# Performance work log

Hardware: AMD Instinct MI355X
Metric: run time of the kernel (lower is better)

The kernel has to match this reference:

```python
import jax, jax.numpy as jnp
import numpy as np

N_HEAD = 16


def setup_inputs() -> dict:
    key = jax.random.key(0)
    k1, k2, k3 = jax.random.split(key, 3)
    B, T, C = 2, 2048, 1024
    x = jax.random.normal(k1, (B, T, C), dtype=jnp.float32)
    w_attn = jax.random.normal(k2, (C, 3 * C), dtype=jnp.float32) * 0.02
    w_proj = jax.random.normal(k3, (C, C), dtype=jnp.float32) * 0.02
    return {"x": x, "w_attn": w_attn, "w_proj": w_proj}


def reference(x, w_attn, w_proj):
    B, T, C = x.shape
    H = N_HEAD
    D = C // H
    qkv = x @ w_attn  # [B, T, 3C]
    q, k, v = jnp.split(qkv, 3, axis=2)
    q = q.reshape(B, T, H, D)
    k = k.reshape(B, T, H, D)
    v = v.reshape(B, T, H, D)
    scale = 1.0 / jnp.sqrt(jnp.asarray(D, dtype=x.dtype))
    # Full T x T score matrix, matching the 'standard_attention' path.
    att = jnp.einsum('bthd,bshd->bhts', q, k) * scale  # [B, H, T, T]
    causal = jnp.tril(jnp.ones((T, T), dtype=bool))
    att = jnp.where(causal[None, None, :, :], att, jnp.asarray(-jnp.inf, dtype=att.dtype))
    att = jax.nn.softmax(att, axis=-1)
    # dropout_p is False (== 0.0) in the original module, so no dropout applied.
    y = jnp.einsum('bhts,bshd->bthd', att, v)  # [B, T, H, D]
    y = y.reshape(B, T, C)
    return y @ w_proj
```

## Files before the change

### kernel.cpp

```cpp
#include <hip/hip_runtime.h>
#include <math.h>

#define BB 2
#define TT 2048
#define HH 16
#define DD 64
#define CC 1024
#define C3 3072

typedef __attribute__((ext_vector_type(8))) short bf16x8;
typedef __attribute__((ext_vector_type(4))) short bf16x4;
typedef __attribute__((ext_vector_type(4))) float f32x4;
typedef __attribute__((ext_vector_type(2))) unsigned int u32x2;

__device__ __forceinline__ unsigned short f2bf(float f) {
  union { float f; unsigned u; } v; v.f = f;
  unsigned r = v.u + 0x7fffu + ((v.u >> 16) & 1u);
  return (unsigned short)(r >> 16);
}
__device__ __forceinline__ unsigned short f2bf_up(float f) {
  union { float f; unsigned u; } v; v.f = f;
  return (unsigned short)((v.u + 0x8000u) >> 16);
}

__device__ __forceinline__ void async_cp16(const void* g, void* l) {
  __builtin_amdgcn_global_load_lds(
      (const __attribute__((address_space(1))) void*)g,
      (__attribute__((address_space(3))) void*)l, 16, 0, 0);
}

__global__ __launch_bounds__(256)
void prep(const float* __restrict__ x, const float* __restrict__ w_attn,
          const float* __restrict__ w_proj, unsigned short* __restrict__ xb,
          unsigned short* __restrict__ wat, unsigned short* __restrict__ wpt) {
  __shared__ __align__(16) float Ts[64][68];
  const int bx = blockIdx.x, tid = threadIdx.x;
  if (bx < 1024) {
    int i = bx * 256 + tid;
#pragma unroll
    for (int it = 0; it < 4; ++it, i += 262144) {
      const float4 v = ((const float4*)x)[i];
      bf16x4 o = {(short)f2bf(v.x), (short)f2bf(v.y),
                  (short)f2bf(v.z), (short)f2bf(v.w)};
      ((bf16x4*)xb)[i] = o;
    }
    return;
  }
  const float* W;
  unsigned short* WT;
  int Nd, bound, n0, k0;
  float s;
  if (bx < 1792) {
    const int bid = bx - 1024;
    W = w_attn; WT = wat; Nd = 3072; bound = 1024; s = 0.18033688f;
    n0 = (bid % 48) * 64; k0 = (bid / 48) * 64;
  } else {
    const int bid = bx - 1792;
    W = w_proj; WT = wpt; Nd = 1024; bound = 0; s = 1.0f;
    n0 = (bid % 16) * 64; k0 = (bid / 16) * 64;
  }
  const int rl = tid >> 4, c4 = tid & 15;
#pragma unroll
  for (int it = 0; it < 4; ++it) {
    const int r = it * 16 + rl;
    *(float4*)&Ts[r][c4 * 4] =
        *(const float4*)(W + (size_t)(k0 + r) * Nd + n0 + c4 * 4);
  }
  __syncthreads();
#pragma unroll
  for (int it = 0; it < 4; ++it) {
    const int n = it * 16 + rl;
    const float sc = (n0 + n < bound) ? s : 1.0f;
    bf16x4 o = {(short)f2bf(Ts[c4 * 4 + 0][n] * sc),
                (short)f2bf(Ts[c4 * 4 + 1][n] * sc),
                (short)f2bf(Ts[c4 * 4 + 2][n] * sc),
                (short)f2bf(Ts[c4 * 4 + 3][n] * sc)};
    *(bf16x4*)(WT + (size_t)(n0 + n) * CC + k0 + c4 * 4) = o;
  }
}

__global__ __launch_bounds__(256, 2)
void gemm_qkv(const unsigned short* __restrict__ A,
              const unsigned short* __restrict__ BT,
              unsigned short* __restrict__ Cb,
              unsigned short* __restrict__ Vout) {
  __shared__ __align__(16) unsigned short As[2 * 128 * 32];
  __shared__ __align__(16) unsigned short Bs[2 * 192 * 32];

  const int tid = threadIdx.x;
  const int w = tid >> 6, lane = tid & 63;
  const int l15 = lane & 15, quad = lane >> 4;
  const int row0 = blockIdx.y * 128, col0 = blockIdx.x * 192;

  const int ca0 = tid, ca1 = tid + 256;
  const int ra0 = ca0 >> 2, ka0 = ((ca0 & 3) ^ ((ca0 >> 3) & 3)) * 8;
  const int ra1 = ca1 >> 2, ka1 = ((ca1 & 3) ^ ((ca1 >> 3) & 3)) * 8;
  const unsigned short* gA0 = A + (size_t)(row0 + ra0) * CC + ka0;
  const unsigned short* gA1 = A + (size_t)(row0 + ra1) * CC + ka1;
  const int cb0 = tid, cb1 = tid + 256, cb2 = tid + 512;
  const int rb0 = cb0 >> 2, kb0 = ((cb0 & 3) ^ ((cb0 >> 3) & 3)) * 8;
  const int rb1 = cb1 >> 2, kb1 = ((cb1 & 3) ^ ((cb1 >> 3) & 3)) * 8;
  const int rb2 = cb2 >> 2, kb2 = ((cb2 & 3) ^ ((cb2 >> 3) & 3)) * 8;
  const unsigned short* gB0 = BT + (size_t)(col0 + rb0) * CC + kb0;
  const unsigned short* gB1 = BT + (size_t)(col0 + rb1) * CC + kb1;
  const unsigned short* gB2 = BT + (size_t)(col0 + rb2) * CC + kb2;
  const int la0 = tid * 16, la1 = tid * 16 + 4096;
  const int lb0 = tid * 16, lb1 = tid * 16 + 4096, lb2 = tid * 16 + 8192;

  const int fro = l15 * 64 + 16 * (quad ^ ((l15 >> 1) & 3));

  f32x4 acc[8][3];
#pragma unroll
  for (int i = 0; i < 8; ++i)
#pragma unroll
    for (int j = 0; j < 3; ++j) acc[i][j] = (f32x4){0.f, 0.f, 0.f, 0.f};

  async_cp16(gA0, (char*)As + la0);
  async_cp16(gA1, (char*)As + la1);
  async_cp16(gB0, (char*)Bs + lb0);
  async_cp16(gB1, (char*)Bs + lb1);
  async_cp16(gB2, (char*)Bs + lb2);

  for (int i = 0; i < 32; ++i) {
    const int cur = i & 1;
    __syncthreads();

    if (i + 1 < 32) {
      const int k1 = (i + 1) * 32;
      const int ab = (cur ^ 1) * 8192, bb = (cur ^ 1) * 12288;
      async_cp16(gA0 + k1, (char*)As + ab + la0);
      async_cp16(gA1 + k1, (char*)As + ab + la1);
      async_cp16(gB0 + k1, (char*)Bs + bb + lb0);
      async_cp16(gB1 + k1, (char*)Bs + bb + lb1);
      async_cp16(gB2 + k1, (char*)Bs + bb + lb2);
    }

    const char* fA = (const char*)As + cur * 8192 + fro;
    const char* fB = (const char*)Bs + cur * 12288 + w * 3072 + fro;

    bf16x8 af[8], bf[3];
#pragma unroll
    for (int mt = 0; mt < 8; ++mt) af[mt] = *(const bf16x8*)(fA + mt * 1024);
#pragma unroll
    for (int nt = 0; nt < 3; ++nt) bf[nt] = *(const bf16x8*)(fB + nt * 1024);
#pragma unroll
    for (int mt = 0; mt < 8; ++mt)
#pragma unroll
      for (int nt = 0; nt < 3; ++nt)
        acc[mt][nt] = __builtin_amdgcn_mfma_f32_16x16x32_bf16(
            af[mt], bf[nt], acc[mt][nt], 0, 0, 0);
  }

#pragma unroll
  for (int mt = 0; mt < 8; ++mt) {
    const int rbase = row0 + mt * 16 + quad * 4;
#pragma unroll
    for (int nt = 0; nt < 3; ++nt) {
      const int colb = col0 + w * 48 + nt * 16;
      if (colb >= 2048) {
        const int bq = rbase >> 11, t0 = rbase & 2047;
        const int d = colb + l15 - 2048;
        bf16x4 o = {(short)f2bf(acc[mt][nt][0]), (short)f2bf(acc[mt][nt][1]),
                    (short)f2bf(acc[mt][nt][2]), (short)f2bf(acc[mt][nt][3])};
        *(bf16x4*)(Vout + (((size_t)(bq << 10) + d) << 11) + t0) = o;
      } else {
        const int col = colb + l15;
#pragma unroll
        for (int r = 0; r < 4; ++r)
          Cb[(size_t)(rbase + r) * C3 + col] = f2bf(acc[mt][nt][r]);
      }
    }
  }
}

__global__ __launch_bounds__(256, 2)
void gemm_out(const unsigned short* __restrict__ A,
              const unsigned short* __restrict__ BT,
              float* __restrict__ Cf) {
  __shared__ __align__(16) unsigned short As[2 * 64 * 64];
  __shared__ __align__(16) unsigned short Bs[2 * 128 * 64];

  const int tid = threadIdx.x;
  const int w = tid >> 6, lane = tid & 63;
  const int l15 = lane & 15, quad = lane >> 4;
  const int wm = w >> 1, wn = w & 1;
  const int row0 = blockIdx.y * 64, col0 = blockIdx.x * 128;

  const int ca0 = tid, ca1 = tid + 256;
  const int ra0 = ca0 >> 3, ka0 = ((ca0 & 7) ^ ((ca0 >> 3) & 7)) * 8;
  const int ra1 = ca1 >> 3, ka1 = ((ca1 & 7) ^ ((ca1 >> 3) & 7)) * 8;
  const unsigned short* gA0 = A + (size_t)(row0 + ra0) * CC + ka0;
  const unsigned short* gA1 = A + (size_t)(row0 + ra1) * CC + ka1;
  const unsigned short* gB[4];
  int lb[4];
#pragma unroll
  for (int t = 0; t < 4; ++t) {
    const int c = tid + t * 256;
    const int rb = c >> 3, kb = ((c & 7) ^ ((c >> 3) & 7)) * 8;
    gB[t] = BT + (size_t)(col0 + rb) * CC + kb;
    lb[t] = c * 16;
  }
  const int la0 = tid * 16, la1 = tid * 16 + 4096;

  const int fro = l15 * 128 + ((quad ^ (l15 & 7)) << 4);

  f32x4 acc[2][4];
#pragma unroll
  for (int i = 0; i < 2; ++i)
#pragma unroll
    for (int j = 0; j < 4; ++j) acc[i][j] = (f32x4){0.f, 0.f, 0.f, 0.f};

  async_cp16(gA0, (char*)As + la0);
  async_cp16(gA1, (char*)As + la1);
#pragma unroll
  for (int t = 0; t < 4; ++t) async_cp16(gB[t], (char*)Bs + lb[t]);

  for (int i = 0; i < 16; ++i) {
    const int cur = i & 1;
    __syncthreads();

    if (i + 1 < 16) {
      const int k1 = (i + 1) * 64;
      const int ab = (cur ^ 1) * 8192, bb = (cur ^ 1) * 16384;
      async_cp16(gA0 + k1, (char*)As + ab + la0);
      async_cp16(gA1 + k1, (char*)As + ab + la1);
#pragma unroll
      for (int t = 0; t < 4; ++t) async_cp16(gB[t] + k1, (char*)Bs + bb + lb[t]);
    }

    const char* fA = (const char*)As + cur * 8192 + wm * 4096 + fro;
    const char* fB = (const char*)Bs + cur * 16384 + wn * 8192 + fro;

#pragma unroll
    for (int kh = 0; kh < 2; ++kh) {
      const int xo = kh * 64;
      bf16x8 af[2], bf[4];
#pragma unroll
      for (int mt = 0; mt < 2; ++mt)
        af[mt] = *(const bf16x8*)(fA + mt * 2048 + ((fro + xo) & 127) - (fro & 127));
#pragma unroll
      for (int nt = 0; nt < 4; ++nt)
        bf[nt] = *(const bf16x8*)(fB + nt * 2048 + ((fro + xo) & 127) - (fro & 127));
#pragma unroll
      for (int mt = 0; mt < 2; ++mt)
#pragma unroll
        for (int nt = 0; nt < 4; ++nt)
          acc[mt][nt] = __builtin_amdgcn_mfma_f32_16x16x32_bf16(
              af[mt], bf[nt], acc[mt][nt], 0, 0, 0);
    }
  }

#pragma unroll
  for (int mt = 0; mt < 2; ++mt) {
    const int rbase = row0 + wm * 32 + mt * 16 + quad * 4;
#pragma unroll
    for (int r = 0; r < 4; ++r) {
      float* cr = Cf + (size_t)(rbase + r) * CC + col0 + wn * 64 + l15;
#pragma unroll
      for (int nt = 0; nt < 4; ++nt) cr[nt * 16] = acc[mt][nt][r];
    }
  }
}

__global__ __launch_bounds__(256)
void attn_mfma(const unsigned short* __restrict__ qkvb,
               const unsigned short* __restrict__ vt,
               unsigned short* __restrict__ y) {
  const int n = blockIdx.x;
  const int bh = (n & 7) + 8 * ((n >> 3) & 3);
  const int qpair = n >> 5;
  const int b = bh >> 4, h = bh & 15;
  const int tid = threadIdx.x;
  const int w = tid >> 6;
  const int lane = tid & 63;
  const int l15 = lane & 15, quad = lane >> 4;

  __shared__ __align__(16) char Kb[2 * 8192];
  __shared__ __align__(16) char Vb[2 * 8192];
  __shared__ __align__(16) unsigned short Ps[4 * 16 * 72];
  unsigned short* psw = Ps + w * 16 * 72;

  const int lr = lane >> 3;
  const int lc = lane & 7;
  const int srcoff = ((lc ^ lr) << 4);
  const char* ksrc = (const char*)qkvb + ((size_t)(b * TT) * C3 + 1024 + h * 64) * 2;
  const char* vsrc = (const char*)vt + ((size_t)(b * HH + h) * DD * TT) * 2;

  const int fro = l15 * 128 + ((quad ^ (l15 & 7)) << 4);

  bf16x8 onesf;
#pragma unroll
  for (int jj = 0; jj < 8; ++jj) onesf[jj] = (short)0x3F80;

  for (int phase = 0; phase < 2; ++phase) {
    const int qt = phase == 0 ? 31 - qpair : qpair;

    if (phase) __syncthreads();

    const unsigned short* qrow =
        qkvb + (size_t)(b * TT + qt * 64 + w * 16 + l15) * C3 + h * DD;
    bf16x8 qf0 = *(const bf16x8*)(qrow + quad * 8);
    bf16x8 qf1 = *(const bf16x8*)(qrow + 32 + quad * 8);

    f32x4 O[4];
#pragma unroll
    for (int dt = 0; dt < 4; ++dt) O[dt] = (f32x4){0.f, 0.f, 0.f, 0.f};
    f32x4 lacc = (f32x4){0.f, 0.f, 0.f, 0.f};

#pragma unroll
    for (int i = 0; i < 2; ++i) {
      async_cp16(ksrc + (size_t)(w * 16 + i * 8 + lr) * (C3 * 2) + srcoff,
                 Kb + w * 2048 + i * 1024);
      async_cp16(vsrc + (size_t)(w * 16 + i * 8 + lr) * (TT * 2) + srcoff,
                 Vb + w * 2048 + i * 1024);
    }

    for (int j = 0; j <= qt; ++j) {
      const int cur = j & 1;
      __syncthreads();

      if (j < qt) {
        const int key1 = (j + 1) * 64;
        char* kd = Kb + (cur ^ 1) * 8192 + w * 2048;
        char* vd = Vb + (cur ^ 1) * 8192 + w * 2048;
#pragma unroll
        for (int i = 0; i < 2; ++i) {
          async_cp16(
              ksrc + (size_t)(key1 + w * 16 + i * 8 + lr) * (C3 * 2) + srcoff,
              kd + i * 1024);
          async_cp16(
              vsrc + (size_t)(w * 16 + i * 8 + lr) * (TT * 2) + key1 * 2 + srcoff,
              vd + i * 1024);
        }
      }

      const char* Kc = Kb + cur * 8192;
      const char* Vc = Vb + cur * 8192;

      f32x4 S[4];
#pragma unroll
      for (int ct = 0; ct < 4; ++ct) {
        bf16x8 k0 = *(const bf16x8*)(Kc + ct * 2048 + fro);
        bf16x8 k1 = *(const bf16x8*)(Kc + ct * 2048 + (fro ^ 64));
        f32x4 z = (f32x4){-12.f, -12.f, -12.f, -12.f};
        z = __builtin_amdgcn_mfma_f32_16x16x32_bf16(k0, qf0, z, 0, 0, 0);
        z = __builtin_amdgcn_mfma_f32_16x16x32_bf16(k1, qf1, z, 0, 0, 0);
        S[ct] = z;
      }

      if (j == qt) {
#pragma unroll
        for (int ct = 0; ct < 4; ++ct)
#pragma unroll
          for (int r = 0; r < 4; ++r)
            if (16 * ct + quad * 4 + r > w * 16 + l15) S[ct][r] = -INFINITY;
      }

#pragma unroll
      for (int ct = 0; ct < 4; ++ct) {
        const unsigned p0 = f2bf_up(exp2f(S[ct][0]));
        const unsigned p1 = f2bf_up(exp2f(S[ct][1]));
        const unsigned p2 = f2bf_up(exp2f(S[ct][2]));
        const unsigned p3 = f2bf_up(exp2f(S[ct][3]));
        u32x2 d;
        d[0] = p0 | (p1 << 16);
        d[1] = p2 | (p3 << 16);
        *(u32x2*)((char*)psw + l15 * 144 + ct * 32 + quad * 8) = d;
      }

      bf16x8 pf0 = *(const bf16x8*)((char*)psw + l15 * 144 + quad * 16);
      bf16x8 pf1 = *(const bf16x8*)((char*)psw + l15 * 144 + 64 + quad * 16);

      lacc = __builtin_amdgcn_mfma_f32_16x16x32_bf16(onesf, pf0, lacc, 0, 0, 0);
      lacc = __builtin_amdgcn_mfma_f32_16x16x32_bf16(onesf, pf1, lacc, 0, 0, 0);
#pragma unroll
      for (int dt = 0; dt < 4; ++dt) {
        bf16x8 v0 = *(const bf16x8*)(Vc + dt * 2048 + fro);
        bf16x8 v1 = *(const bf16x8*)(Vc + dt * 2048 + (fro ^ 64));
        O[dt] = __builtin_amdgcn_mfma_f32_16x16x32_bf16(v0, pf0, O[dt], 0, 0, 0);
        O[dt] = __builtin_amdgcn_mfma_f32_16x16x32_bf16(v1, pf1, O[dt], 0, 0, 0);
      }
    }

    const float inv = 1.0f / lacc[0];
    unsigned short* yr =
        y + (size_t)(b * TT + qt * 64 + w * 16 + l15) * CC + h * DD + quad * 4;
#pragma unroll
    for (int dt = 0; dt < 4; ++dt) {
      bf16x4 o = {(short)f2bf(O[dt][0] * inv), (short)f2bf(O[dt][1] * inv),
                  (short)f2bf(O[dt][2] * inv), (short)f2bf(O[dt][3] * inv)};
      *(bf16x4*)(yr + dt * 16) = o;
    }
  }
}

extern "C" void kernel_launch(void* const* d_in, const int* in_sizes, int n_in,
                              void* d_out, int out_size, void* d_ws,
                              size_t ws_size, hipStream_t stream) {
  const float* x      = (const float*)d_in[0];
  const float* w_attn = (const float*)d_in[1];
  const float* w_proj = (const float*)d_in[2];
  float* out = (float*)d_out;

  unsigned short* xb   = (unsigned short*)d_ws;
  unsigned short* wat  = xb + (size_t)4096 * 1024;
  unsigned short* wpt  = wat + (size_t)3072 * 1024;
  unsigned short* qkvb = wpt + (size_t)1024 * 1024;
  unsigned short* vt   = qkvb + (size_t)4096 * 3072;
  unsigned short* yb   = vt + (size_t)BB * HH * DD * TT;

  dim3 blk(256);

  prep<<<2048, blk, 0, stream>>>(x, w_attn, w_proj, xb, wat, wpt);

  gemm_qkv<<<dim3(C3 / 192, (BB * TT) / 128), blk, 0, stream>>>(
      xb, wat, qkvb, vt);

  attn_mfma<<<dim3(512, 1, 1), blk, 0, stream>>>(qkvb, vt, yb);

  gemm_out<<<dim3(CC / 128, (BB * TT) / 64), blk, 0, stream>>>(yb, wpt, out);
}
```

Measured before the change: 184.1 us.

## Retile QKV GEMM to 128x128 2x2 warps, swizzle P buffer, use hardware exp2

The QKV GEMM moves from 128x192 tiles with each warp covering all rows to 128x128 tiles on a 2x2 warp grid. This cuts accumulator registers and LDS so three blocks can share a CU, and it raises the block count from 512 to 768. The V-transpose versus row-store choice is now made once per block. In attention, P is packed with the hardware bf16x2 convert and exp2 uses the raw builtin. P tile columns are rotated per row to reduce LDS bank conflicts, and rounding changes from round-up to round-to-nearest.

```diff
diff --git a/kernel.cpp b/kernel.cpp
--- a/kernel.cpp
+++ b/kernel.cpp
@@ -1,4 +1,5 @@
 #include <hip/hip_runtime.h>
+#include <hip/hip_bf16.h>
 #include <math.h>
 
 #define BB 2
@@ -18,9 +19,10 @@
   unsigned r = v.u + 0x7fffu + ((v.u >> 16) & 1u);
   return (unsigned short)(r >> 16);
 }
-__device__ __forceinline__ unsigned short f2bf_up(float f) {
-  union { float f; unsigned u; } v; v.f = f;
-  return (unsigned short)((v.u + 0x8000u) >> 16);
+__device__ __forceinline__ unsigned pack2bf(float a, float b) {
+  __hip_bfloat162 h = __float22bfloat162_rn(make_float2(a, b));
+  union { __hip_bfloat162 h; unsigned u; } cv; cv.h = h;
+  return cv.u;
 }
 
 __device__ __forceinline__ void async_cp16(const void* g, void* l) {
@@ -79,47 +81,41 @@
   }
 }
 
-__global__ __launch_bounds__(256, 2)
+__global__ __launch_bounds__(256, 3)
 void gemm_qkv(const unsigned short* __restrict__ A,
               const unsigned short* __restrict__ BT,
               unsigned short* __restrict__ Cb,
               unsigned short* __restrict__ Vout) {
   __shared__ __align__(16) unsigned short As[2 * 128 * 32];
-  __shared__ __align__(16) unsigned short Bs[2 * 192 * 32];
+  __shared__ __align__(16) unsigned short Bs[2 * 128 * 32];
 
   const int tid = threadIdx.x;
   const int w = tid >> 6, lane = tid & 63;
   const int l15 = lane & 15, quad = lane >> 4;
-  const int row0 = blockIdx.y * 128, col0 = blockIdx.x * 192;
+  const int wm = w >> 1, wn = w & 1;
+  const int row0 = blockIdx.y * 128, col0 = blockIdx.x * 128;
 
   const int ca0 = tid, ca1 = tid + 256;
   const int ra0 = ca0 >> 2, ka0 = ((ca0 & 3) ^ ((ca0 >> 3) & 3)) * 8;
   const int ra1 = ca1 >> 2, ka1 = ((ca1 & 3) ^ ((ca1 >> 3) & 3)) * 8;
   const unsigned short* gA0 = A + (size_t)(row0 + ra0) * CC + ka0;
   const unsigned short* gA1 = A + (size_t)(row0 + ra1) * CC + ka1;
-  const int cb0 = tid, cb1 = tid + 256, cb2 = tid + 512;
-  const int rb0 = cb0 >> 2, kb0 = ((cb0 & 3) ^ ((cb0 >> 3) & 3)) * 8;
-  const int rb1 = cb1 >> 2, kb1 = ((cb1 & 3) ^ ((cb1 >> 3) & 3)) * 8;
-  const int rb2 = cb2 >> 2, kb2 = ((cb2 & 3) ^ ((cb2 >> 3) & 3)) * 8;
-  const unsigned short* gB0 = BT + (size_t)(col0 + rb0) * CC + kb0;
-  const unsigned short* gB1 = BT + (size_t)(col0 + rb1) * CC + kb1;
-  const unsigned short* gB2 = BT + (size_t)(col0 + rb2) * CC + kb2;
+  const unsigned short* gB0 = BT + (size_t)(col0 + ra0) * CC + ka0;
+  const unsigned short* gB1 = BT + (size_t)(col0 + ra1) * CC + ka1;
   const int la0 = tid * 16, la1 = tid * 16 + 4096;
-  const int lb0 = tid * 16, lb1 = tid * 16 + 4096, lb2 = tid * 16 + 8192;
 
   const int fro = l15 * 64 + 16 * (quad ^ ((l15 >> 1) & 3));
 
-  f32x4 acc[8][3];
-#pragma unroll
-  for (int i = 0; i < 8; ++i)
-#pragma unroll
-    for (int j = 0; j < 3; ++j) acc[i][j] = (f32x4){0.f, 0.f, 0.f, 0.f};
+  f32x4 acc[4][4];
+#pragma unroll
+  for (int i = 0; i < 4; ++i)
+#pragma unroll
+    for (int j = 0; j < 4; ++j) acc[i][j] = (f32x4){0.f, 0.f, 0.f, 0.f};
 
   async_cp16(gA0, (char*)As + la0);
   async_cp16(gA1, (char*)As + la1);
-  async_cp16(gB0, (char*)Bs + lb0);
-  async_cp16(gB1, (char*)Bs + lb1);
-  async_cp16(gB2, (char*)Bs + lb2);
+  async_cp16(gB0, (char*)Bs + la0);
+  async_cp16(gB1, (char*)Bs + la1);
 
   for (int i = 0; i < 32; ++i) {
     const int cur = i & 1;
@@ -127,47 +123,52 @@
 
     if (i + 1 < 32) {
       const int k1 = (i + 1) * 32;
-      const int ab = (cur ^ 1) * 8192, bb = (cur ^ 1) * 12288;
+      const int ab = (cur ^ 1) * 8192;
       async_cp16(gA0 + k1, (char*)As + ab + la0);
       async_cp16(gA1 + k1, (char*)As + ab + la1);
-      async_cp16(gB0 + k1, (char*)Bs + bb + lb0);
-      async_cp16(gB1 + k1, (char*)Bs + bb + lb1);
-      async_cp16(gB2 + k1, (char*)Bs + bb + lb2);
-    }
-
-    const char* fA = (const char*)As + cur * 8192 + fro;
-    const char* fB = (const char*)Bs + cur * 12288 + w * 3072 + fro;
-
-    bf16x8 af[8], bf[3];
-#pragma unroll
-    for (int mt = 0; mt < 8; ++mt) af[mt] = *(const bf16x8*)(fA + mt * 1024);
-#pragma unroll
-    for (int nt = 0; nt < 3; ++nt) bf[nt] = *(const bf16x8*)(fB + nt * 1024);
-#pragma unroll
-    for (int mt = 0; mt < 8; ++mt)
-#pragma unroll
-      for (int nt = 0; nt < 3; ++nt)
+      async_cp16(gB0 + k1, (char*)Bs + ab + la0);
+      async_cp16(gB1 + k1, (char*)Bs + ab + la1);
+    }
+
+    const char* fA = (const char*)As + cur * 8192 + wm * 4096 + fro;
+    const char* fB = (const char*)Bs + cur * 8192 + wn * 4096 + fro;
+
+    bf16x8 af[4], bf[4];
+#pragma unroll
+    for (int mt = 0; mt < 4; ++mt) af[mt] = *(const bf16x8*)(fA + mt * 1024);
+#pragma unroll
+    for (int nt = 0; nt < 4; ++nt) bf[nt] = *(const bf16x8*)(fB + nt * 1024);
+#pragma unroll
+    for (int mt = 0; mt < 4; ++mt)
+#pragma unroll
+      for (int nt = 0; nt < 4; ++nt)
         acc[mt][nt] = __builtin_amdgcn_mfma_f32_16x16x32_bf16(
             af[mt], bf[nt], acc[mt][nt], 0, 0, 0);
   }
 
-#pragma unroll
-  for (int mt = 0; mt < 8; ++mt) {
-    const int rbase = row0 + mt * 16 + quad * 4;
-#pragma unroll
-    for (int nt = 0; nt < 3; ++nt) {
-      const int colb = col0 + w * 48 + nt * 16;
-      if (colb >= 2048) {
-        const int bq = rbase >> 11, t0 = rbase & 2047;
-        const int d = colb + l15 - 2048;
+  if (col0 >= 2048) {
+#pragma unroll
+    for (int mt = 0; mt < 4; ++mt) {
+      const int rbase = row0 + wm * 64 + mt * 16 + quad * 4;
+      const int bq = rbase >> 11, t0 = rbase & 2047;
+#pragma unroll
+      for (int nt = 0; nt < 4; ++nt) {
+        const int d = col0 + wn * 64 + nt * 16 + l15 - 2048;
         bf16x4 o = {(short)f2bf(acc[mt][nt][0]), (short)f2bf(acc[mt][nt][1]),
                     (short)f2bf(acc[mt][nt][2]), (short)f2bf(acc[mt][nt][3])};
         *(bf16x4*)(Vout + (((size_t)(bq << 10) + d) << 11) + t0) = o;
-      } else {
-        const int col = colb + l15;
-#pragma unroll
-        for (int r = 0; r < 4; ++r)
-          Cb[(size_t)(rbase + r) * C3 + col] = f2bf(acc[mt][nt][r]);
+      }
+    }
+  } else {
+#pragma unroll
+    for (int mt = 0; mt < 4; ++mt) {
+      const int rbase = row0 + wm * 64 + mt * 16 + quad * 4;
+#pragma unroll
+      for (int r = 0; r < 4; ++r) {
+        unsigned short* cr =
+            Cb + (size_t)(rbase + r) * C3 + col0 + wn * 64 + l15;
+#pragma unroll
+        for (int nt = 0; nt < 4; ++nt) cr[nt * 16] = f2bf(acc[mt][nt][r]);
       }
     }
   }
@@ -278,7 +279,7 @@
   __shared__ __align__(16) char Kb[2 * 8192];
   __shared__ __align__(16) char Vb[2 * 8192];
   __shared__ __align__(16) unsigned short Ps[4 * 16 * 72];
-  unsigned short* psw = Ps + w * 16 * 72;
+  char* psw = (char*)(Ps + w * 16 * 72);
 
   const int lr = lane >> 3;
   const int lc = lane & 7;
@@ -287,6 +288,8 @@
   const char* vsrc = (const char*)vt + ((size_t)(b * HH + h) * DD * TT) * 2;
 
   const int fro = l15 * 128 + ((quad ^ (l15 & 7)) << 4);
+
+  const int psrow = l15 * 144;
 
   bf16x8 onesf;
 #pragma unroll
@@ -358,18 +361,20 @@
 
 #pragma unroll
       for (int ct = 0; ct < 4; ++ct) {
-        const unsigned p0 = f2bf_up(exp2f(S[ct][0]));
-        const unsigned p1 = f2bf_up(exp2f(S[ct][1]));
-        const unsigned p2 = f2bf_up(exp2f(S[ct][2]));
-        const unsigned p3 = f2bf_up(exp2f(S[ct][3]));
         u32x2 d;
-        d[0] = p0 | (p1 << 16);
-        d[1] = p2 | (p3 << 16);
-        *(u32x2*)((char*)psw + l15 * 144 + ct * 32 + quad * 8) = d;
-      }
-
-      bf16x8 pf0 = *(const bf16x8*)((char*)psw + l15 * 144 + quad * 16);
-      bf16x8 pf1 = *(const bf16x8*)((char*)psw + l15 * 144 + 64 + quad * 16);
+        d[0] = pack2bf(__builtin_amdgcn_exp2f(S[ct][0]),
+                       __builtin_amdgcn_exp2f(S[ct][1]));
+        d[1] = pack2bf(__builtin_amdgcn_exp2f(S[ct][2]),
+                       __builtin_amdgcn_exp2f(S[ct][3]));
+        *(u32x2*)(psw + psrow + (((ct + l15) & 3) << 5) + quad * 8) = d;
+      }
+
+      bf16x8 pf0, pf1;
+      {
+        const int c0 = (quad >> 1), c1 = 2 + (quad >> 1);
+        pf0 = *(const bf16x8*)(psw + psrow + (((c0 + l15) & 3) << 5) + ((quad & 1) << 4));
+        pf1 = *(const bf16x8*)(psw + psrow + (((c1 + l15) & 3) << 5) + ((quad & 1) << 4));
+      }
 
       lacc = __builtin_amdgcn_mfma_f32_16x16x32_bf16(onesf, pf0, lacc, 0, 0, 0);
       lacc = __builtin_amdgcn_mfma_f32_16x16x32_bf16(onesf, pf1, lacc, 0, 0, 0);
@@ -413,7 +418,7 @@
 
   prep<<<2048, blk, 0, stream>>>(x, w_attn, w_proj, xb, wat, wpt);
 
-  gemm_qkv<<<dim3(C3 / 192, (BB * TT) / 128), blk, 0, stream>>>(
+  gemm_qkv<<<dim3(C3 / 128, (BB * TT) / 128), blk, 0, stream>>>(
       xb, wat, qkvb, vt);
 
   attn_mfma<<<dim3(512, 1, 1), blk, 0, stream>>>(qkvb, vt, yb);
```

Result: faster. 171.7 us (-6.7%).
